# Optimization experiments

Measured on AMD Instinct MI355X. Metric: run time of the kernel, lower is better.

The kernel has to match this reference:

```python
import jax, jax.numpy as jnp
import numpy as np

N_NODES = 5000
N_EDGES = 40000
NUM_ATOM_TYPES = 100
HID = 32            # multiplicity of 0e and 1o in irreps_hidden
EDGE_ATTR_DIM = 8
NUM_BOND_TYPES = 5
OUT_SCALARS = 2 * 6 + 1  # max_charge=6 -> 13x0e
CUTOFF = 5.0
SQRT3 = 1.7320508075688772


def _sh(edge_vec):
    # o3.SphericalHarmonics('1x0e + 1x1o', normalize=True, normalization='component')
    d = jnp.sqrt(jnp.sum(edge_vec * edge_vec, axis=-1) + 1e-12)
    n = edge_vec / d[:, None]
    sh0 = jnp.ones(edge_vec.shape[0], edge_vec.dtype)          # [E]
    sh1 = SQRT3 * n[:, (1, 2, 0)]                              # [E,3], e3nn (y,z,x) order
    return sh0, sh1, d


def _soft_one_hot(d):
    # e3nn.math.soft_one_hot_linspace(d, 0, cutoff, 8, basis='gaussian', cutoff=True)
    values = jnp.linspace(0.0, CUTOFF, EDGE_ATTR_DIM + 2)[1:-1]
    step = CUTOFF / (EDGE_ATTR_DIM + 1)
    diff = (d[:, None] - values[None, :]) / step
    return jnp.exp(-diff * diff) / 1.12


def _mlp(x, W0, b0, W1, b1):
    # ScalarMLP(in, out, hidden=[in], SiLU)
    return jax.nn.silu(x @ W0 + b0) @ W1 + b1


def _tp_init(s, sh0, sh1, w):
    # FCTP(32x0e, 1x0e+1x1o -> 32x0e+32x1o); paths: 0e*0e->0e, 0e*1o->1o
    E = s.shape[0]
    w1 = w[:, : HID * HID].reshape(E, HID, HID)
    w2 = w[:, HID * HID :].reshape(E, HID, HID)
    c = 1.0 / np.sqrt(HID)  # fan-in = 32 per output irrep
    out_s = c * jnp.einsum('eu,euw->ew', s * sh0[:, None], w1)
    out_v = c * jnp.einsum('eu,ei,euw->ewi', s, sh1, w2)
    return out_s, out_v


def _tp_hidden(s, v, sh0, sh1, w):
    # FCTP(32x0e+32x1o, 1x0e+1x1o -> 32x0e+32x1o)
    # path order: 0e*0e->0e, 0e*1o->1o, 1o*0e->1o, 1o*1o->0e
    E = s.shape[0]
    ws = w.reshape(E, 4, HID, HID)
    c = 1.0 / np.sqrt(2 * HID)  # fan-in = 64 per output irrep
    dot = jnp.einsum('eui,ei->eu', v, sh1) / SQRT3  # CG(1,1->0) = delta/sqrt(3)
    out_s = c * (jnp.einsum('eu,euw->ew', s * sh0[:, None], ws[:, 0]) +
                 jnp.einsum('eu,euw->ew', dot, ws[:, 3]))
    out_v = c * (jnp.einsum('eu,ei,euw->ewi', s, sh1, ws[:, 1]) +
                 jnp.einsum('eui,euw->ewi', v * sh0[:, None, None], ws[:, 2]))
    return out_s, out_v


def _edge_tp(s1, v1, s2, v2, sh0, sh1, w):
    # FCTP(64x0e+64x1o (concat of two hidden), 1x0e+1x1o -> 5x0e)
    # blocks in concat order: s_src, v_src, s_dst, v_dst
    E = s1.shape[0]
    ws = w.reshape(E, 4, HID, NUM_BOND_TYPES)
    c = 1.0 / np.sqrt(4 * HID)  # fan-in = 128
    d1 = jnp.einsum('eui,ei->eu', v1, sh1) / SQRT3
    d2 = jnp.einsum('eui,ei->eu', v2, sh1) / SQRT3
    return c * (jnp.einsum('eu,euw->ew', s1 * sh0[:, None], ws[:, 0]) +
                jnp.einsum('eu,euw->ew', d1, ws[:, 1]) +
                jnp.einsum('eu,euw->ew', s2 * sh0[:, None], ws[:, 2]) +
                jnp.einsum('eu,euw->ew', d2, ws[:, 3]))


def _scatter_mean(ms, mv, dst, n):
    cnt = jax.ops.segment_sum(jnp.ones(dst.shape[0], ms.dtype), dst, num_segments=n)
    cnt = jnp.maximum(cnt, 1.0)
    s = jax.ops.segment_sum(ms, dst, num_segments=n) / cnt[:, None]
    v = jax.ops.segment_sum(mv, dst, num_segments=n) / cnt[:, None, None]
    return s, v


def setup_inputs() -> dict:
    key = jax.random.key(0)
    ks = jax.random.split(key, 16)
    def w(k, shape, fan_in):
        return jax.random.normal(k, shape, dtype=jnp.float32) / np.sqrt(fan_in)
    inp = {}
    inp['coordinates'] = jax.random.normal(ks[0], (N_NODES, 3), dtype=jnp.float32) * 1.5
    inp['atom_types'] = jax.random.randint(ks[1], (N_NODES,), 0, NUM_ATOM_TYPES)
    inp['edge_index'] = jax.random.randint(ks[2], (2, N_EDGES), 0, N_NODES)
    inp['atom_embed'] = jax.random.normal(ks[3], (NUM_ATOM_TYPES, HID), dtype=jnp.float32)
    inp['ip_W0'] = w(ks[4], (EDGE_ATTR_DIM, EDGE_ATTR_DIM), EDGE_ATTR_DIM)
    inp['ip_b0'] = jnp.zeros((EDGE_ATTR_DIM,), jnp.float32)
    inp['ip_W1'] = w(ks[5], (EDGE_ATTR_DIM, 2 * HID * HID), EDGE_ATTR_DIM)
    inp['ip_b1'] = jnp.zeros((2 * HID * HID,), jnp.float32)
    inp['ly_W0'] = w(ks[6], (EDGE_ATTR_DIM, EDGE_ATTR_DIM), EDGE_ATTR_DIM)
    inp['ly_b0'] = jnp.zeros((EDGE_ATTR_DIM,), jnp.float32)
    inp['ly_W1'] = w(ks[7], (EDGE_ATTR_DIM, 4 * HID * HID), EDGE_ATTR_DIM)
    inp['ly_b1'] = jnp.zeros((4 * HID * HID,), jnp.float32)
    inp['ly_Ws'] = jax.random.normal(ks[8], (HID, HID), dtype=jnp.float32)
    inp['ly_Wv'] = jax.random.normal(ks[9], (HID, HID), dtype=jnp.float32)
    inp['et_W0'] = w(ks[10], (EDGE_ATTR_DIM, EDGE_ATTR_DIM), EDGE_ATTR_DIM)
    inp['et_b0'] = jnp.zeros((EDGE_ATTR_DIM,), jnp.float32)
    inp['et_W1'] = w(ks[11], (EDGE_ATTR_DIM, 4 * HID * NUM_BOND_TYPES), EDGE_ATTR_DIM)
    inp['et_b1'] = jnp.zeros((4 * HID * NUM_BOND_TYPES,), jnp.float32)
    inp['no_W1'] = jax.random.normal(ks[12], (HID, OUT_SCALARS), dtype=jnp.float32)
    inp['no_W2'] = jax.random.normal(ks[13], (OUT_SCALARS, OUT_SCALARS), dtype=jnp.float32)
    return inp


def reference(coordinates, atom_types, edge_index, atom_embed,
              ip_W0, ip_b0, ip_W1, ip_b1,
              ly_W0, ly_b0, ly_W1, ly_b1, ly_Ws, ly_Wv,
              et_W0, et_b0, et_W1, et_b1, no_W1, no_W2):
    n = coordinates.shape[0]
    src, dst = edge_index[0], edge_index[1]
    edge_vec = coordinates[dst] - coordinates[src]
    sh0, sh1, d = _sh(edge_vec)
    edge_attr = _soft_one_hot(d)                              # [E,8]
    # initial projector: Conv(32x0e -> 32x0e+32x1o)
    s0 = atom_embed[atom_types]                               # [N,32]
    w_ip = _mlp(edge_attr, ip_W0, ip_b0, ip_W1, ip_b1)        # [E,2048]
    ms, mv = _tp_init(s0[src], sh0, sh1, w_ip)
    s, v = _scatter_mean(ms, mv, dst, n)                      # [N,32],[N,32,3]
    # one LinearSelfInteraction(Conv) layer
    w_ly = _mlp(edge_attr, ly_W0, ly_b0, ly_W1, ly_b1)        # [E,4096]
    ms, mv = _tp_hidden(s[src], v[src], sh0, sh1, w_ly)
    cs, cv = _scatter_mean(ms, mv, dst, n)
    lc = 1.0 / np.sqrt(HID)  # e3nn o3.Linear normalization
    s = cs + lc * (s @ ly_Ws)
    v = cv + lc * jnp.einsum('eui,uw->ewi', v, ly_Wv)
    # edge output: FCTP([h_src, h_dst], edge_sh) with radial weights
    w_et = _mlp(edge_attr, et_W0, et_b0, et_W1, et_b1)        # [E,640]
    edge_out = _edge_tp(s[src], v[src], s[dst], v[dst], sh0, sh1, w_et)  # [E,5]
    # node output MLP on detached scalar channel (13x0e)
    sd = jax.lax.stop_gradient(s)
    h = jax.nn.silu(sd @ no_W1 / np.sqrt(HID))
    node_out = h @ no_W2 / np.sqrt(OUT_SCALARS)               # [N,13]
    return edge_out, node_out
```

## Files before the change

kernel.cpp:

```cpp
#include <hip/hip_runtime.h>

#define NN 5000
#define NE 40000

typedef unsigned int u32;
typedef unsigned short u16;
typedef __fp16 h16x2 __attribute__((ext_vector_type(2)));
typedef _Float16 f16x8 __attribute__((ext_vector_type(8)));
typedef __attribute__((ext_vector_type(4))) float f32x4;

union AF { u32 u[4]; f16x8 v; uint4 q; };

__device__ __forceinline__ float siluf(float x) { return x / (1.f + __expf(-x)); }

__device__ __forceinline__ u32 f2bf_u(float f) {
  u32 x = __float_as_uint(f);
  return (x + 0x7FFFu + ((x >> 16) & 1u)) >> 16;
}
__device__ __forceinline__ u16 f2bf(float f) { return (u16)f2bf_u(f); }
__device__ __forceinline__ u32 packbf2(float lo, float hi) {
  return f2bf_u(lo) | (f2bf_u(hi) << 16);
}
__device__ __forceinline__ u32 pkh2(float a, float b) {
  union { h16x2 h; u32 u; } r;
  r.h = __builtin_amdgcn_cvt_pkrtz(a, b);
  return r.u;
}
__device__ __forceinline__ u16 f2h(float v) {
  _Float16 h = (_Float16)v;
  return *(u16*)&h;
}
__device__ __forceinline__ void unpack8(uint4 q, float* f) {
  f[0] = __uint_as_float(q.x << 16); f[1] = __uint_as_float(q.x & 0xFFFF0000u);
  f[2] = __uint_as_float(q.y << 16); f[3] = __uint_as_float(q.y & 0xFFFF0000u);
  f[4] = __uint_as_float(q.z << 16); f[5] = __uint_as_float(q.z & 0xFFFF0000u);
  f[6] = __uint_as_float(q.w << 16); f[7] = __uint_as_float(q.w & 0xFFFF0000u);
}
__device__ __forceinline__ float dot8f(const float* h, const float* w, float init) {
  float a = init;
#pragma unroll
  for (int k = 0; k < 8; k++) a = fmaf(h[k], w[k], a);
  return a;
}
__device__ __forceinline__ void mlp8(const float* ea, const float* __restrict__ W0,
                                     const float* __restrict__ b0, float* h) {
#pragma unroll
  for (int j = 0; j < 8; j++) {
    float a = b0[j];
#pragma unroll
    for (int i = 0; i < 8; i++) a += ea[i] * W0[i*8 + j];
    h[j] = siluf(a);
  }
}
__device__ __forceinline__ AF mkfrag(float hs, const float* s) {
  AF a;
  a.u[0] = pkh2(hs*s[0], hs*s[1]);
  a.u[1] = pkh2(hs*s[2], hs*s[3]);
  a.u[2] = pkh2(hs*s[4], hs*s[5]);
  a.u[3] = pkh2(hs*s[6], hs*s[7]);
  return a;
}

__global__ __launch_bounds__(256) void k_prep(
    const float* __restrict__ ipW1, const float* __restrict__ ipb1,
    const float* __restrict__ lyW1, const float* __restrict__ lyb1,
    u16* __restrict__ ipT, u16* __restrict__ lyT) {
  int b = blockIdx.x;
  if (b < 16) {
    int h = b >> 3;
    int t0 = (b & 7)*2304 + threadIdx.x*9;
#pragma unroll
    for (int j = 0; j < 9; j++) {
      int t = t0 + j;
      int kch = t >> 9, rem = t & 511;
      int col = rem >> 3, kk = rem & 7;
      int k = kch*8 + kk;
      int basec = (h == 0) ? ((col >> 5)*1024 + (col & 31))
                           : ((col < 32) ? (2048 + col) : (3072 + (col - 32)));
      float v = (k < 256) ? lyW1[(k >> 5)*4096 + basec + (k & 31)*32]
                          : lyb1[basec + (k - 256)*32];
      lyT[h*18432 + t] = f2h(v);
    }
  } else {
    int t0 = (b - 16)*2304 + threadIdx.x*9;
#pragma unroll
    for (int j = 0; j < 9; j++) {
      int t = t0 + j;
      int kch = t >> 9, rem = t & 511;
      int col = rem >> 3, kk = rem & 7;
      int k = kch*8 + kk;
      int pth = col >> 5, w = col & 31;
      float v = (k < 256) ? ipW1[(k >> 5)*2048 + pth*1024 + (k & 31)*32 + w]
                          : ipb1[pth*1024 + (k - 256)*32 + w];
      ipT[t] = f2h(v);
    }
  }
}

__global__ __launch_bounds__(256) void k_conv1(
    const float* __restrict__ coords, const int* __restrict__ eidx,
    const float* __restrict__ emb, const int* __restrict__ atype,
    const float* __restrict__ ipW0, const float* __restrict__ ipb0,
    const float* __restrict__ lyW0, const float* __restrict__ lyb0,
    const float* __restrict__ etW0, const float* __restrict__ etb0,
    const u16* __restrict__ ipT,
    float* __restrict__ sh, float* __restrict__ h_ly, float* __restrict__ h_et,
    int* __restrict__ cur, int* __restrict__ perm, u16* __restrict__ msg) {
  int wid = threadIdx.x >> 6, lane = threadIdx.x & 63;
  int tile = blockIdx.x*4 + wid;
  int m = lane & 15, q = lane >> 4;
  int e = tile*16 + m;
  int s = eidx[e], d = eidx[NE + e];
  float vx = coords[d*3+0] - coords[s*3+0];
  float vy = coords[d*3+1] - coords[s*3+1];
  float vz = coords[d*3+2] - coords[s*3+2];
  float dist = sqrtf(vx*vx + vy*vy + vz*vz + 1e-12f);
  float dinv = 1.f / dist;
  const float SQ3 = 1.7320508075688772f;
  float sh0 = SQ3 * vy * dinv;
  float sh1 = SQ3 * vz * dinv;
  float sh2 = SQ3 * vx * dinv;
  int srow = atype[s];
  float ea[8];
  const float step = 5.f / 9.f;
#pragma unroll
  for (int jj = 0; jj < 8; jj++) {
    float diff = (dist - step * (float)(jj+1)) * (9.f / 5.f);
    ea[jj] = __expf(-diff*diff) * (1.f / 1.12f);
  }
  float hip[8], hly[8], het[8];
  mlp8(ea, ipW0, ipb0, hip);
  mlp8(ea, lyW0, lyb0, hly);
  mlp8(ea, etW0, etb0, het);
  if (q == 0) {
    sh[e*3+0] = sh0; sh[e*3+1] = sh1; sh[e*3+2] = sh2;
    { float4 f0 = {hly[0],hly[1],hly[2],hly[3]}, f1 = {hly[4],hly[5],hly[6],hly[7]};
      *(float4*)&h_ly[e*8] = f0; *(float4*)&h_ly[e*8+4] = f1; }
    { float4 f0 = {het[0],het[1],het[2],het[3]}, f1 = {het[4],het[5],het[6],het[7]};
      *(float4*)&h_et[e*8] = f0; *(float4*)&h_et[e*8+4] = f1; }
    int* cp = &cur[d];
    atomicCAS(cp, (int)0xAAAAAAAA, 0);
    int t = atomicAdd(cp, 1);
    if (t < 64) perm[d*64 + t] = e;
  }
  float4 sA = *(const float4*)&emb[srow*32 + q*8];
  float4 sB = *(const float4*)&emb[srow*32 + q*8 + 4];
  float sf[8] = {sA.x,sA.y,sA.z,sA.w,sB.x,sB.y,sB.z,sB.w};
  f32x4 acc0 = {0.f,0.f,0.f,0.f}, acc1 = acc0, acc2 = acc0, acc3 = acc0;
  const float cs = 0.17677669529663687f;
#pragma unroll
  for (int ks = 0; ks < 9; ks++) {
    float hs = (ks < 8) ? hip[ks] : 1.f;
    AF a = mkfrag(hs, sf);
    int c2 = (ks*4 + q)*64;
    AF b0, b1f, b2, b3;
    b0.q  = *(const uint4*)&ipT[(c2 +  0 + m)*8];
    b1f.q = *(const uint4*)&ipT[(c2 + 16 + m)*8];
    b2.q  = *(const uint4*)&ipT[(c2 + 32 + m)*8];
    b3.q  = *(const uint4*)&ipT[(c2 + 48 + m)*8];
    acc0 = __builtin_amdgcn_mfma_f32_16x16x32_f16(a.v, b0.v,  acc0, 0, 0, 0);
    acc1 = __builtin_amdgcn_mfma_f32_16x16x32_f16(a.v, b1f.v, acc1, 0, 0, 0);
    acc2 = __builtin_amdgcn_mfma_f32_16x16x32_f16(a.v, b2.v,  acc2, 0, 0, 0);
    acc3 = __builtin_amdgcn_mfma_f32_16x16x32_f16(a.v, b3.v,  acc3, 0, 0, 0);
  }
#pragma unroll
  for (int r = 0; r < 4; r++) {
    int et = tile*16 + q*4 + r;
    u16* mp = msg + (size_t)et*128;
    mp[m]      = f2bf(cs*acc0[r]);
    mp[16 + m] = f2bf(cs*acc1[r]);
    float s0v = __shfl(sh0, q*4 + r, 64);
    float s1v = __shfl(sh1, q*4 + r, 64);
    float s2v = __shfl(sh2, q*4 + r, 64);
    float m0 = cs*acc2[r], m1 = cs*acc3[r];
    mp[32 +      m] = f2bf(m0*s0v);
    mp[64 +      m] = f2bf(m0*s1v);
    mp[96 +      m] = f2bf(m0*s2v);
    mp[32 + 16 + m] = f2bf(m1*s0v);
    mp[64 + 16 + m] = f2bf(m1*s1v);
    mp[96 + 16 + m] = f2bf(m1*s2v);
  }
}

__global__ __launch_bounds__(256) void k_conv2(
    const float* __restrict__ hE, const float* __restrict__ sh,
    const float* __restrict__ s1, const float* __restrict__ v1soa,
    const int* __restrict__ eidx, const u16* __restrict__ lyT,
    u16* __restrict__ msgA, u16* __restrict__ msgB) {
  int wid = threadIdx.x >> 6, lane = threadIdx.x & 63;
  const bool scalarHalf = blockIdx.x < 625;
  int blk = scalarHalf ? blockIdx.x : blockIdx.x - 625;
  int tile = blk*4 + wid;
  int m = lane & 15, q = lane >> 4;
  const u16* Bg = lyT + (scalarHalf ? 0 : 18432);
  const float c = 0.125f;
  int e = tile*16 + m;
  int srcn = eidx[e];
  float4 hA = *(const float4*)&hE[e*8];
  float4 hB = *(const float4*)&hE[e*8 + 4];
  float hf[8] = {hA.x,hA.y,hA.z,hA.w,hB.x,hB.y,hB.z,hB.w};

  if (scalarHalf) {
    float4 sA = *(const float4*)&s1[srcn*32 + q*8];
    float4 sB = *(const float4*)&s1[srcn*32 + q*8 + 4];
    float sf[8] = {sA.x,sA.y,sA.z,sA.w,sB.x,sB.y,sB.z,sB.w};
    f32x4 acc0 = {0.f,0.f,0.f,0.f}, acc1 = acc0, acc2 = acc0, acc3 = acc0;
#pragma unroll
    for (int ks = 0; ks < 9; ks++) {
      float hs = (ks < 8) ? hf[ks] : 1.f;
      AF a = mkfrag(hs, sf);
      int c2 = (ks*4 + q)*64;
      AF b0, b1f, b2, b3;
      b0.q  = *(const uint4*)&Bg[(c2 +  0 + m)*8];
      b1f.q = *(const uint4*)&Bg[(c2 + 16 + m)*8];
      b2.q  = *(const uint4*)&Bg[(c2 + 32 + m)*8];
      b3.q  = *(const uint4*)&Bg[(c2 + 48 + m)*8];
      acc0 = __builtin_amdgcn_mfma_f32_16x16x32_f16(a.v, b0.v,  acc0, 0, 0, 0);
      acc1 = __builtin_amdgcn_mfma_f32_16x16x32_f16(a.v, b1f.v, acc1, 0, 0, 0);
      acc2 = __builtin_amdgcn_mfma_f32_16x16x32_f16(a.v, b2.v,  acc2, 0, 0, 0);
      acc3 = __builtin_amdgcn_mfma_f32_16x16x32_f16(a.v, b3.v,  acc3, 0, 0, 0);
    }
#pragma unroll
    for (int r = 0; r < 4; r++) {
      int et = tile*16 + q*4 + r;
      u16* mp = msgA + (size_t)et*128;
      mp[m]      = f2bf(c*acc0[r]);
      mp[16 + m] = f2bf(c*acc1[r]);
      float s0v = sh[et*3+0], s1v = sh[et*3+1], s2v = sh[et*3+2];
      float m0 = c*acc2[r], m1 = c*acc3[r];
      mp[32 +      m] = f2bf(m0*s0v);
      mp[64 +      m] = f2bf(m0*s1v);
      mp[96 +      m] = f2bf(m0*s2v);
      mp[32 + 16 + m] = f2bf(m1*s0v);
      mp[64 + 16 + m] = f2bf(m1*s1v);
      mp[96 + 16 + m] = f2bf(m1*s2v);
    }
  } else {
    const float is3 = 0.5773502691896258f;
    float vf[3][8];
#pragma unroll
    for (int i = 0; i < 3; i++) {
      float4 aa = *(const float4*)&v1soa[i*160000 + srcn*32 + q*8];
      float4 bb = *(const float4*)&v1soa[i*160000 + srcn*32 + q*8 + 4];
      vf[i][0]=aa.x; vf[i][1]=aa.y; vf[i][2]=aa.z; vf[i][3]=aa.w;
      vf[i][4]=bb.x; vf[i][5]=bb.y; vf[i][6]=bb.z; vf[i][7]=bb.w;
    }
    float es0 = sh[e*3+0], es1 = sh[e*3+1], es2 = sh[e*3+2];
    float df[8];
#pragma unroll
    for (int j = 0; j < 8; j++)
      df[j] = (vf[0][j]*es0 + vf[1][j]*es1 + vf[2][j]*es2) * is3;
    f32x4 z = {0.f,0.f,0.f,0.f};
    f32x4 aV00 = z, aV01 = z, aV10 = z, aV11 = z, aV20 = z, aV21 = z, aD0 = z, aD1 = z;
#pragma unroll
    for (int ks = 0; ks < 9; ks++) {
      float hs = (ks < 8) ? hf[ks] : 1.f;
      int c2 = (ks*4 + q)*64;
      AF b0, b1f, b2, b3;
      b0.q  = *(const uint4*)&Bg[(c2 +  0 + m)*8];
      b1f.q = *(const uint4*)&Bg[(c2 + 16 + m)*8];
      b2.q  = *(const uint4*)&Bg[(c2 + 32 + m)*8];
      b3.q  = *(const uint4*)&Bg[(c2 + 48 + m)*8];
      AF a0 = mkfrag(hs, vf[0]);
      AF a1 = mkfrag(hs, vf[1]);
      AF a2 = mkfrag(hs, vf[2]);
      AF ad = mkfrag(hs, df);
      aV00 = __builtin_amdgcn_mfma_f32_16x16x32_f16(a0.v, b0.v,  aV00, 0, 0, 0);
      aV01 = __builtin_amdgcn_mfma_f32_16x16x32_f16(a0.v, b1f.v, aV01, 0, 0, 0);
      aV10 = __builtin_amdgcn_mfma_f32_16x16x32_f16(a1.v, b0.v,  aV10, 0, 0, 0);
      aV11 = __builtin_amdgcn_mfma_f32_16x16x32_f16(a1.v, b1f.v, aV11, 0, 0, 0);
      aV20 = __builtin_amdgcn_mfma_f32_16x16x32_f16(a2.v, b0.v,  aV20, 0, 0, 0);
      aV21 = __builtin_amdgcn_mfma_f32_16x16x32_f16(a2.v, b1f.v, aV21, 0, 0, 0);
      aD0  = __builtin_amdgcn_mfma_f32_16x16x32_f16(ad.v, b2.v,  aD0,  0, 0, 0);
      aD1  = __builtin_amdgcn_mfma_f32_16x16x32_f16(ad.v, b3.v,  aD1,  0, 0, 0);
    }
#pragma unroll
    for (int r = 0; r < 4; r++) {
      int et = tile*16 + q*4 + r;
      u16* mp = msgB + (size_t)et*128;
      mp[m]      = f2bf(c*aD0[r]);
      mp[16 + m] = f2bf(c*aD1[r]);
      mp[32 +      m] = f2bf(c*aV00[r]);
      mp[32 + 16 + m] = f2bf(c*aV01[r]);
      mp[64 +      m] = f2bf(c*aV10[r]);
      mp[64 + 16 + m] = f2bf(c*aV11[r]);
      mp[96 +      m] = f2bf(c*aV20[r]);
      mp[96 + 16 + m] = f2bf(c*aV21[r]);
    }
  }
}

__global__ __launch_bounds__(256) void k_gather1(
    const u16* __restrict__ msg, const int* __restrict__ perm,
    const int* __restrict__ cur, float* __restrict__ s1,
    float* __restrict__ v1soa) {
  __shared__ int pe[2][64];
  int ln = threadIdx.x >> 7, c = threadIdx.x & 127;
  int n = blockIdx.x*2 + ln;
  int deg = min(cur[n], 64);
  if (c < 64) pe[ln][c] = perm[n*64 + c];
  __syncthreads();
  float acc = 0.f;
  int j = 0;
  for (; j + 4 <= deg; j += 4) {
    int e0 = pe[ln][j], e1 = pe[ln][j+1], e2 = pe[ln][j+2], e3 = pe[ln][j+3];
    float x0 = __uint_as_float(((u32)msg[(size_t)e0*128 + c]) << 16);
    float x1 = __uint_as_float(((u32)msg[(size_t)e1*128 + c]) << 16);
    float x2 = __uint_as_float(((u32)msg[(size_t)e2*128 + c]) << 16);
    float x3 = __uint_as_float(((u32)msg[(size_t)e3*128 + c]) << 16);
    acc += (x0 + x1) + (x2 + x3);
  }
  for (; j < deg; j++)
    acc += __uint_as_float(((u32)msg[(size_t)pe[ln][j]*128 + c]) << 16);
  acc /= (float)max(deg, 1);
  if (c < 32) s1[n*32 + c] = acc;
  else { int i = (c-32) >> 5, w = (c-32) & 31; v1soa[i*160000 + n*32 + w] = acc; }
}

__global__ __launch_bounds__(256) void k_gather2(
    const u16* __restrict__ msgA, const u16* __restrict__ msgB,
    const int* __restrict__ perm, const int* __restrict__ cur,
    const float* __restrict__ s1, const float* __restrict__ v1soa,
    const float* __restrict__ Ws, const float* __restrict__ Wv,
    const float* __restrict__ noW1, const float* __restrict__ noW2,
    float* __restrict__ s2, float* __restrict__ v2, float* __restrict__ outN) {
  __shared__ int pe[2][64];
  __shared__ float sb[2][32];
  __shared__ float hb[2][13];
  int ln = threadIdx.x >> 7, c = threadIdx.x & 127;
  int n = blockIdx.x*2 + ln;
  int deg = min(cur[n], 64);
  if (c < 64) pe[ln][c] = perm[n*64 + c];
  __syncthreads();
  float acc = 0.f;
  int j = 0;
  for (; j + 4 <= deg; j += 4) {
    int e0 = pe[ln][j], e1 = pe[ln][j+1], e2 = pe[ln][j+2], e3 = pe[ln][j+3];
    float x0 = __uint_as_float(((u32)msgA[(size_t)e0*128 + c]) << 16)
             + __uint_as_float(((u32)msgB[(size_t)e0*128 + c]) << 16);
    float x1 = __uint_as_float(((u32)msgA[(size_t)e1*128 + c]) << 16)
             + __uint_as_float(((u32)msgB[(size_t)e1*128 + c]) << 16);
    float x2 = __uint_as_float(((u32)msgA[(size_t)e2*128 + c]) << 16)
             + __uint_as_float(((u32)msgB[(size_t)e2*128 + c]) << 16);
    float x3 = __uint_as_float(((u32)msgA[(size_t)e3*128 + c]) << 16)
             + __uint_as_float(((u32)msgB[(size_t)e3*128 + c]) << 16);
    acc += (x0 + x1) + (x2 + x3);
  }
  for (; j < deg; j++) {
    int e = pe[ln][j];
    acc += __uint_as_float(((u32)msgA[(size_t)e*128 + c]) << 16)
         + __uint_as_float(((u32)msgB[(size_t)e*128 + c]) << 16);
  }
  acc /= (float)max(deg, 1);
  const float lc = 0.17677669529663687f;
  if (c < 32) {
    float ss = 0.f;
#pragma unroll 8
    for (int u = 0; u < 32; u++) ss += s1[n*32 + u] * Ws[u*32 + c];
    float val = acc + lc*ss;
    s2[n*32 + c] = val;
    sb[ln][c] = val;
  } else {
    int i = (c-32) >> 5, w = (c-32) & 31;
    float sv = 0.f;
#pragma unroll 8
    for (int u = 0; u < 32; u++) sv += v1soa[i*160000 + n*32 + u] * Wv[u*32 + w];
    v2[n*96 + w*3 + i] = acc + lc*sv;
  }
  __syncthreads();
  const float i32 = 0.17677669529663687f;
  if (c < 13) {
    float a = 0.f;
#pragma unroll 8
    for (int u = 0; u < 32; u++) a += sb[ln][u] * noW1[u*13 + c];
    hb[ln][c] = siluf(a * i32);
  }
  __syncthreads();
  const float i13 = 0.2773500981126146f;
  if (c < 13) {
    float a = 0.f;
#pragma unroll
    for (int j2 = 0; j2 < 13; j2++) a += hb[ln][j2] * noW2[j2*13 + c];
    outN[n*13 + c] = a * i13;
  }
}

__global__ __launch_bounds__(256) void k_e3(
    const float* __restrict__ hE, const float* __restrict__ sh,
    const float* __restrict__ s2, const float* __restrict__ v2,
    const int* __restrict__ eidx,
    const float* __restrict__ W1, const float* __restrict__ b1,
    float* __restrict__ out) {
  __shared__ uint4 WQ[640];
  __shared__ float BQ[640];
  for (int t = threadIdx.x; t < 640; t += 256) {
    int u = t & 31, pw = t >> 5, p2 = pw / 5, w = pw - p2*5;
    int col = p2*160 + u*5 + w;
    const float* s = W1 + col;
    uint4 q;
    q.x = packbf2(s[0],      s[640]);
    q.y = packbf2(s[1280],   s[1920]);
    q.z = packbf2(s[2560],   s[3200]);
    q.w = packbf2(s[3840],   s[4480]);
    WQ[t] = q;
    BQ[t] = b1[col];
  }
  __syncthreads();
  const int g = threadIdx.x >> 5, tw = threadIdx.x & 31;
  const float c = 0.08838834764831845f;
  const float is3 = 0.5773502691896258f;
  for (int p = blockIdx.x*8 + g; p*2 < NE; p += gridDim.x*8) {
    int e0 = p*2, e1 = e0 + 1;
    float h0[8], h1[8];
    {
      float4 qa = *(const float4*)&hE[e0*8];
      float4 qb = *(const float4*)&hE[e0*8+4];
      h0[0]=qa.x; h0[1]=qa.y; h0[2]=qa.z; h0[3]=qa.w;
      h0[4]=qb.x; h0[5]=qb.y; h0[6]=qb.z; h0[7]=qb.w;
      float4 qc = *(const float4*)&hE[e1*8];
      float4 qd = *(const float4*)&hE[e1*8+4];
      h1[0]=qc.x; h1[1]=qc.y; h1[2]=qc.z; h1[3]=qc.w;
      h1[4]=qd.x; h1[5]=qd.y; h1[6]=qd.z; h1[7]=qd.w;
    }
    int sA = eidx[e0], dA = eidx[NE+e0];
    int sB = eidx[e1], dB = eidx[NE+e1];
    float sa0 = sh[e0*3+0], sa1 = sh[e0*3+1], sa2 = sh[e0*3+2];
    float sb0 = sh[e1*3+0], sb1 = sh[e1*3+1], sb2 = sh[e1*3+2];
    float c00 = s2[sA*32 + tw];
    float c01 = (v2[sA*96+tw*3+0]*sa0 + v2[sA*96+tw*3+1]*sa1 + v2[sA*96+tw*3+2]*sa2) * is3;
    float c02 = s2[dA*32 + tw];
    float c03 = (v2[dA*96+tw*3+0]*sa0 + v2[dA*96+tw*3+1]*sa1 + v2[dA*96+tw*3+2]*sa2) * is3;
    float c10 = s2[sB*32 + tw];
    float c11 = (v2[sB*96+tw*3+0]*sb0 + v2[sB*96+tw*3+1]*sb1 + v2[sB*96+tw*3+2]*sb2) * is3;
    float c12 = s2[dB*32 + tw];
    float c13 = (v2[dB*96+tw*3+0]*sb0 + v2[dB*96+tw*3+1]*sb1 + v2[dB*96+tw*3+2]*sb2) * is3;
    float part0[5] = {0,0,0,0,0};
    float part1[5] = {0,0,0,0,0};
#pragma unroll
    for (int pp = 0; pp < 4; pp++) {
      float cp0 = (pp==0) ? c00 : (pp==1) ? c01 : (pp==2) ? c02 : c03;
      float cp1 = (pp==0) ? c10 : (pp==1) ? c11 : (pp==2) ? c12 : c13;
#pragma unroll
      for (int w = 0; w < 5; w++) {
        int idx = (pp*5 + w)*32 + tw;
        float f[8];
        unpack8(WQ[idx], f);
        float bv = BQ[idx];
        part0[w] = fmaf(cp0, dot8f(h0, f, bv), part0[w]);
        part1[w] = fmaf(cp1, dot8f(h1, f, bv), part1[w]);
      }
    }
#pragma unroll
    for (int off = 16; off > 0; off >>= 1)
#pragma unroll
      for (int w = 0; w < 5; w++) {
        part0[w] += __shfl_xor(part0[w], off, 32);
        part1[w] += __shfl_xor(part1[w], off, 32);
      }
    float outv = 0.f;
#pragma unroll
    for (int w = 0; w < 5; w++) {
      if (tw == w)     outv = part0[w];
      if (tw == 5 + w) outv = part1[w];
    }
    if (tw < 10) out[e0*5 + tw] = c * outv;
  }
}

extern "C" void kernel_launch(void* const* d_in, const int* in_sizes, int n_in,
                              void* d_out, int out_size, void* d_ws, size_t ws_size,
                              hipStream_t stream) {
  (void)in_sizes; (void)n_in; (void)out_size; (void)ws_size;
  const float* coords = (const float*)d_in[0];
  const int*   atype  = (const int*)d_in[1];
  const int*   eidx   = (const int*)d_in[2];
  const float* emb    = (const float*)d_in[3];
  const float* ipW0 = (const float*)d_in[4];
  const float* ipb0 = (const float*)d_in[5];
  const float* ipW1 = (const float*)d_in[6];
  const float* ipb1 = (const float*)d_in[7];
  const float* lyW0 = (const float*)d_in[8];
  const float* lyb0 = (const float*)d_in[9];
  const float* lyW1 = (const float*)d_in[10];
  const float* lyb1 = (const float*)d_in[11];
  const float* lyWs = (const float*)d_in[12];
  const float* lyWv = (const float*)d_in[13];
  const float* etW0 = (const float*)d_in[14];
  const float* etb0 = (const float*)d_in[15];
  const float* etW1 = (const float*)d_in[16];
  const float* etb1 = (const float*)d_in[17];
  const float* noW1 = (const float*)d_in[18];
  const float* noW2 = (const float*)d_in[19];

  float* ws = (float*)d_ws;
  float* sh    = ws;
  float* h_ly  = ws + 440000;
  float* h_et  = ws + 760000;
  float* s1    = ws + 1240000;
  float* v1soa = ws + 1400000;
  float* s2    = ws + 1880000;
  float* v2    = ws + 2040000;
  int*   cur   = (int*)(ws + 2520000);
  int*   perm  = (int*)(ws + 2525000);
  u16*   msgA  = (u16*)(ws + 2845000);
  u16*   msgB  = (u16*)(ws + 5405000);
  u16*   lyT   = (u16*)(ws + 7965000);
  u16*   ipT   = (u16*)(ws + 7983432);

  float* outE = (float*)d_out;
  float* outN = (float*)d_out + NE*5;

  k_prep<<<24, 256, 0, stream>>>(ipW1, ipb1, lyW1, lyb1, ipT, lyT);
  k_conv1<<<625, 256, 0, stream>>>(coords, eidx, emb, atype,
                                   ipW0, ipb0, lyW0, lyb0, etW0, etb0,
                                   ipT, sh, h_ly, h_et, cur, perm, msgA);
  k_gather1<<<NN/2, 256, 0, stream>>>(msgA, perm, cur, s1, v1soa);
  k_conv2<<<1250, 256, 0, stream>>>(h_ly, sh, s1, v1soa, eidx, lyT, msgA, msgB);
  k_gather2<<<NN/2, 256, 0, stream>>>(msgA, msgB, perm, cur, s1, v1soa,
                                      lyWs, lyWv, noW1, noW2, s2, v2, outN);
  k_e3<<<1024, 256, 0, stream>>>(h_et, sh, s2, v2, eidx, etW1, etb1, outE);
}
```

Measured before the change: 164.9 us.

## Write messages directly into per-destination slots and stage weights in LDS

Conv kernels now write each edge message straight into a dense per-destination slot buffer indexed by (dst, atomic slot), so the gather kernels read contiguous rows without a perm indirection. Message components are interleaved per channel (s, vx, vy, vz) and stored with packed 8-byte writes instead of scattered 2-byte stores. The k_prep launch is removed: each conv block converts its slice of W1/b1 to fp16 in shared memory, which adds per-block redundant conversion work and a large LDS footprint that may limit occupancy. The message buffers grow to NN*64 slots each, so more workspace is touched.

```diff
diff --git a/kernel.cpp b/kernel.cpp
--- a/kernel.cpp
+++ b/kernel.cpp
@@ -17,7 +17,6 @@
   u32 x = __float_as_uint(f);
   return (x + 0x7FFFu + ((x >> 16) & 1u)) >> 16;
 }
-__device__ __forceinline__ u16 f2bf(float f) { return (u16)f2bf_u(f); }
 __device__ __forceinline__ u32 packbf2(float lo, float hi) {
   return f2bf_u(lo) | (f2bf_u(hi) << 16);
 }
@@ -60,42 +59,7 @@
   a.u[3] = pkh2(hs*s[6], hs*s[7]);
   return a;
 }
-
-__global__ __launch_bounds__(256) void k_prep(
-    const float* __restrict__ ipW1, const float* __restrict__ ipb1,
-    const float* __restrict__ lyW1, const float* __restrict__ lyb1,
-    u16* __restrict__ ipT, u16* __restrict__ lyT) {
-  int b = blockIdx.x;
-  if (b < 16) {
-    int h = b >> 3;
-    int t0 = (b & 7)*2304 + threadIdx.x*9;
-#pragma unroll
-    for (int j = 0; j < 9; j++) {
-      int t = t0 + j;
-      int kch = t >> 9, rem = t & 511;
-      int col = rem >> 3, kk = rem & 7;
-      int k = kch*8 + kk;
-      int basec = (h == 0) ? ((col >> 5)*1024 + (col & 31))
-                           : ((col < 32) ? (2048 + col) : (3072 + (col - 32)));
-      float v = (k < 256) ? lyW1[(k >> 5)*4096 + basec + (k & 31)*32]
-                          : lyb1[basec + (k - 256)*32];
-      lyT[h*18432 + t] = f2h(v);
-    }
-  } else {
-    int t0 = (b - 16)*2304 + threadIdx.x*9;
-#pragma unroll
-    for (int j = 0; j < 9; j++) {
-      int t = t0 + j;
-      int kch = t >> 9, rem = t & 511;
-      int col = rem >> 3, kk = rem & 7;
-      int k = kch*8 + kk;
-      int pth = col >> 5, w = col & 31;
-      float v = (k < 256) ? ipW1[(k >> 5)*2048 + pth*1024 + (k & 31)*32 + w]
-                          : ipb1[pth*1024 + (k - 256)*32 + w];
-      ipT[t] = f2h(v);
-    }
-  }
-}
+__device__ __forceinline__ float bf2f(u16 v) { return __uint_as_float(((u32)v) << 16); }
 
 __global__ __launch_bounds__(256) void k_conv1(
     const float* __restrict__ coords, const int* __restrict__ eidx,
@@ -103,9 +67,19 @@
     const float* __restrict__ ipW0, const float* __restrict__ ipb0,
     const float* __restrict__ lyW0, const float* __restrict__ lyb0,
     const float* __restrict__ etW0, const float* __restrict__ etb0,
-    const u16* __restrict__ ipT,
+    const float* __restrict__ ipW1, const float* __restrict__ ipb1,
     float* __restrict__ sh, float* __restrict__ h_ly, float* __restrict__ h_et,
-    int* __restrict__ cur, int* __restrict__ perm, u16* __restrict__ msg) {
+    int* __restrict__ cur, int* __restrict__ slot, u16* __restrict__ msg) {
+  __shared__ __align__(16) u16 B2[18432];
+  {
+    int col = threadIdx.x & 63, pth = col >> 5, w = col & 31;
+    int k0 = (threadIdx.x >> 6) * 72;
+    for (int k = k0; k < k0 + 72; k++) {
+      float v = (k < 256) ? ipW1[(k >> 5)*2048 + pth*1024 + (k & 31)*32 + w]
+                          : ipb1[pth*1024 + (k - 256)*32 + w];
+      B2[((k >> 3)*64 + col)*8 + (k & 7)] = f2h(v);
+    }
+  }
   int wid = threadIdx.x >> 6, lane = threadIdx.x & 63;
   int tile = blockIdx.x*4 + wid;
   int m = lane & 15, q = lane >> 4;
@@ -132,6 +106,7 @@
   mlp8(ea, ipW0, ipb0, hip);
   mlp8(ea, lyW0, lyb0, hly);
   mlp8(ea, etW0, etb0, het);
+  int t = 0;
   if (q == 0) {
     sh[e*3+0] = sh0; sh[e*3+1] = sh1; sh[e*3+2] = sh2;
     { float4 f0 = {hly[0],hly[1],hly[2],hly[3]}, f1 = {hly[4],hly[5],hly[6],hly[7]};
@@ -140,12 +115,13 @@
       *(float4*)&h_et[e*8] = f0; *(float4*)&h_et[e*8+4] = f1; }
     int* cp = &cur[d];
     atomicCAS(cp, (int)0xAAAAAAAA, 0);
-    int t = atomicAdd(cp, 1);
-    if (t < 64) perm[d*64 + t] = e;
+    t = atomicAdd(cp, 1);
+    slot[e] = t;
   }
   float4 sA = *(const float4*)&emb[srow*32 + q*8];
   float4 sB = *(const float4*)&emb[srow*32 + q*8 + 4];
   float sf[8] = {sA.x,sA.y,sA.z,sA.w,sB.x,sB.y,sB.z,sB.w};
+  __syncthreads();
   f32x4 acc0 = {0.f,0.f,0.f,0.f}, acc1 = acc0, acc2 = acc0, acc3 = acc0;
   const float cs = 0.17677669529663687f;
 #pragma unroll
@@ -154,10 +130,10 @@
     AF a = mkfrag(hs, sf);
     int c2 = (ks*4 + q)*64;
     AF b0, b1f, b2, b3;
-    b0.q  = *(const uint4*)&ipT[(c2 +  0 + m)*8];
-    b1f.q = *(const uint4*)&ipT[(c2 + 16 + m)*8];
-    b2.q  = *(const uint4*)&ipT[(c2 + 32 + m)*8];
-    b3.q  = *(const uint4*)&ipT[(c2 + 48 + m)*8];
+    b0.q  = *(const uint4*)&B2[(c2 +  0 + m)*8];
+    b1f.q = *(const uint4*)&B2[(c2 + 16 + m)*8];
+    b2.q  = *(const uint4*)&B2[(c2 + 32 + m)*8];
+    b3.q  = *(const uint4*)&B2[(c2 + 48 + m)*8];
     acc0 = __builtin_amdgcn_mfma_f32_16x16x32_f16(a.v, b0.v,  acc0, 0, 0, 0);
     acc1 = __builtin_amdgcn_mfma_f32_16x16x32_f16(a.v, b1f.v, acc1, 0, 0, 0);
     acc2 = __builtin_amdgcn_mfma_f32_16x16x32_f16(a.v, b2.v,  acc2, 0, 0, 0);
@@ -165,40 +141,79 @@
   }
 #pragma unroll
   for (int r = 0; r < 4; r++) {
-    int et = tile*16 + q*4 + r;
-    u16* mp = msg + (size_t)et*128;
-    mp[m]      = f2bf(cs*acc0[r]);
-    mp[16 + m] = f2bf(cs*acc1[r]);
-    float s0v = __shfl(sh0, q*4 + r, 64);
-    float s1v = __shfl(sh1, q*4 + r, 64);
-    float s2v = __shfl(sh2, q*4 + r, 64);
-    float m0 = cs*acc2[r], m1 = cs*acc3[r];
-    mp[32 +      m] = f2bf(m0*s0v);
-    mp[64 +      m] = f2bf(m0*s1v);
-    mp[96 +      m] = f2bf(m0*s2v);
-    mp[32 + 16 + m] = f2bf(m1*s0v);
-    mp[64 + 16 + m] = f2bf(m1*s1v);
-    mp[96 + 16 + m] = f2bf(m1*s2v);
-  }
+    int L = q*4 + r;
+    int tE = __shfl(t, L, 64);
+    int dn = __shfl(d, L, 64);
+    float s0v = __shfl(sh0, L, 64);
+    float s1v = __shfl(sh1, L, 64);
+    float s2v = __shfl(sh2, L, 64);
+    if (tE < 64) {
+      u16* mp = msg + ((size_t)dn*64 + tE)*128;
+      float m0 = cs*acc2[r], m1 = cs*acc3[r];
+      uint2 p0 = { packbf2(cs*acc0[r], m0*s0v), packbf2(m0*s1v, m0*s2v) };
+      *(uint2*)&mp[m*4] = p0;
+      uint2 p1 = { packbf2(cs*acc1[r], m1*s0v), packbf2(m1*s1v, m1*s2v) };
+      *(uint2*)&mp[64 + m*4] = p1;
+    }
+  }
+}
+
+__global__ __launch_bounds__(256) void k_gather1(
+    const u16* __restrict__ msg, const int* __restrict__ cur,
+    float* __restrict__ s1, float* __restrict__ v1soa) {
+  int ln = threadIdx.x >> 7, c = threadIdx.x & 127;
+  int n = blockIdx.x*2 + ln;
+  int deg = min(cur[n], 64);
+  const u16* base = msg + (size_t)n*64*128 + c;
+  float acc = 0.f;
+  int j = 0;
+  for (; j + 4 <= deg; j += 4) {
+    float x0 = bf2f(base[(j+0)*128]);
+    float x1 = bf2f(base[(j+1)*128]);
+    float x2 = bf2f(base[(j+2)*128]);
+    float x3 = bf2f(base[(j+3)*128]);
+    acc += (x0 + x1) + (x2 + x3);
+  }
+  for (; j < deg; j++) acc += bf2f(base[j*128]);
+  acc /= (float)max(deg, 1);
+  int col = c >> 2, comp = c & 3;
+  if (comp == 0) s1[n*32 + col] = acc;
+  else           v1soa[(comp-1)*160000 + n*32 + col] = acc;
 }
 
 __global__ __launch_bounds__(256) void k_conv2(
     const float* __restrict__ hE, const float* __restrict__ sh,
     const float* __restrict__ s1, const float* __restrict__ v1soa,
-    const int* __restrict__ eidx, const u16* __restrict__ lyT,
+    const int* __restrict__ eidx, const int* __restrict__ slot,
+    const float* __restrict__ lyW1, const float* __restrict__ lyb1,
     u16* __restrict__ msgA, u16* __restrict__ msgB) {
-  int wid = threadIdx.x >> 6, lane = threadIdx.x & 63;
+  __shared__ __align__(16) u16 B2[18432];
   const bool scalarHalf = blockIdx.x < 625;
   int blk = scalarHalf ? blockIdx.x : blockIdx.x - 625;
+  {
+    int col = threadIdx.x & 63;
+    int k0 = (threadIdx.x >> 6) * 72;
+    int basec = scalarHalf ? ((col >> 5)*1024 + (col & 31))
+                           : ((col < 32) ? (2048 + col) : (3072 + (col - 32)));
+    for (int k = k0; k < k0 + 72; k++) {
+      float v = (k < 256) ? lyW1[(k >> 5)*4096 + basec + (k & 31)*32]
+                          : lyb1[basec + (k - 256)*32];
+      B2[((k >> 3)*64 + col)*8 + (k & 7)] = f2h(v);
+    }
+  }
+  int wid = threadIdx.x >> 6, lane = threadIdx.x & 63;
   int tile = blk*4 + wid;
   int m = lane & 15, q = lane >> 4;
-  const u16* Bg = lyT + (scalarHalf ? 0 : 18432);
   const float c = 0.125f;
   int e = tile*16 + m;
   int srcn = eidx[e];
+  int dnv  = eidx[NE + e];
+  int slv  = slot[e];
+  float s0p = sh[e*3+0], s1p = sh[e*3+1], s2p = sh[e*3+2];
   float4 hA = *(const float4*)&hE[e*8];
   float4 hB = *(const float4*)&hE[e*8 + 4];
   float hf[8] = {hA.x,hA.y,hA.z,hA.w,hB.x,hB.y,hB.z,hB.w};
+  __syncthreads();
 
   if (scalarHalf) {
     float4 sA = *(const float4*)&s1[srcn*32 + q*8];
@@ -211,10 +226,10 @@
       AF a = mkfrag(hs, sf);
       int c2 = (ks*4 + q)*64;
       AF b0, b1f, b2, b3;
-      b0.q  = *(const uint4*)&Bg[(c2 +  0 + m)*8];
-      b1f.q = *(const uint4*)&Bg[(c2 + 16 + m)*8];
-      b2.q  = *(const uint4*)&Bg[(c2 + 32 + m)*8];
-      b3.q  = *(const uint4*)&Bg[(c2 + 48 + m)*8];
+      b0.q  = *(const uint4*)&B2[(c2 +  0 + m)*8];
+      b1f.q = *(const uint4*)&B2[(c2 + 16 + m)*8];
+      b2.q  = *(const uint4*)&B2[(c2 + 32 + m)*8];
+      b3.q  = *(const uint4*)&B2[(c2 + 48 + m)*8];
       acc0 = __builtin_amdgcn_mfma_f32_16x16x32_f16(a.v, b0.v,  acc0, 0, 0, 0);
       acc1 = __builtin_amdgcn_mfma_f32_16x16x32_f16(a.v, b1f.v, acc1, 0, 0, 0);
       acc2 = __builtin_amdgcn_mfma_f32_16x16x32_f16(a.v, b2.v,  acc2, 0, 0, 0);
@@ -222,18 +237,20 @@
     }
 #pragma unroll
     for (int r = 0; r < 4; r++) {
-      int et = tile*16 + q*4 + r;
-      u16* mp = msgA + (size_t)et*128;
-      mp[m]      = f2bf(c*acc0[r]);
-      mp[16 + m] = f2bf(c*acc1[r]);
-      float s0v = sh[et*3+0], s1v = sh[et*3+1], s2v = sh[et*3+2];
-      float m0 = c*acc2[r], m1 = c*acc3[r];
-      mp[32 +      m] = f2bf(m0*s0v);
-      mp[64 +      m] = f2bf(m0*s1v);
-      mp[96 +      m] = f2bf(m0*s2v);
-      mp[32 + 16 + m] = f2bf(m1*s0v);
-      mp[64 + 16 + m] = f2bf(m1*s1v);
-      mp[96 + 16 + m] = f2bf(m1*s2v);
+      int L = q*4 + r;
+      int tE = __shfl(slv, L, 64);
+      int dn = __shfl(dnv, L, 64);
+      float s0v = __shfl(s0p, L, 64);
+      float s1v = __shfl(s1p, L, 64);
+      float s2v = __shfl(s2p, L, 64);
+      if (tE < 64) {
+        u16* mp = msgA + ((size_t)dn*64 + tE)*128;
+        float m0 = c*acc2[r], m1 = c*acc3[r];
+        uint2 p0 = { packbf2(c*acc0[r], m0*s0v), packbf2(m0*s1v, m0*s2v) };
+        *(uint2*)&mp[m*4] = p0;
+        uint2 p1 = { packbf2(c*acc1[r], m1*s0v), packbf2(m1*s1v, m1*s2v) };
+        *(uint2*)&mp[64 + m*4] = p1;
+      }
     }
   } else {
     const float is3 = 0.5773502691896258f;
@@ -245,11 +262,10 @@
       vf[i][0]=aa.x; vf[i][1]=aa.y; vf[i][2]=aa.z; vf[i][3]=aa.w;
       vf[i][4]=bb.x; vf[i][5]=bb.y; vf[i][6]=bb.z; vf[i][7]=bb.w;
     }
-    float es0 = sh[e*3+0], es1 = sh[e*3+1], es2 = sh[e*3+2];
     float df[8];
 #pragma unroll
     for (int j = 0; j < 8; j++)
-      df[j] = (vf[0][j]*es0 + vf[1][j]*es1 + vf[2][j]*es2) * is3;
+      df[j] = (vf[0][j]*s0p + vf[1][j]*s1p + vf[2][j]*s2p) * is3;
     f32x4 z = {0.f,0.f,0.f,0.f};
     f32x4 aV00 = z, aV01 = z, aV10 = z, aV11 = z, aV20 = z, aV21 = z, aD0 = z, aD1 = z;
 #pragma unroll
@@ -257,10 +273,10 @@
       float hs = (ks < 8) ? hf[ks] : 1.f;
       int c2 = (ks*4 + q)*64;
       AF b0, b1f, b2, b3;
-      b0.q  = *(const uint4*)&Bg[(c2 +  0 + m)*8];
-      b1f.q = *(const uint4*)&Bg[(c2 + 16 + m)*8];
-      b2.q  = *(const uint4*)&Bg[(c2 + 32 + m)*8];
-      b3.q  = *(const uint4*)&Bg[(c2 + 48 + m)*8];
+      b0.q  = *(const uint4*)&B2[(c2 +  0 + m)*8];
+      b1f.q = *(const uint4*)&B2[(c2 + 16 + m)*8];
+      b2.q  = *(const uint4*)&B2[(c2 + 32 + m)*8];
+      b3.q  = *(const uint4*)&B2[(c2 + 48 + m)*8];
       AF a0 = mkfrag(hs, vf[0]);
       AF a1 = mkfrag(hs, vf[1]);
       AF a2 = mkfrag(hs, vf[2]);
@@ -276,96 +292,60 @@
     }
 #pragma unroll
     for (int r = 0; r < 4; r++) {
-      int et = tile*16 + q*4 + r;
-      u16* mp = msgB + (size_t)et*128;
-      mp[m]      = f2bf(c*aD0[r]);
-      mp[16 + m] = f2bf(c*aD1[r]);
-      mp[32 +      m] = f2bf(c*aV00[r]);
-      mp[32 + 16 + m] = f2bf(c*aV01[r]);
-      mp[64 +      m] = f2bf(c*aV10[r]);
-      mp[64 + 16 + m] = f2bf(c*aV11[r]);
-      mp[96 +      m] = f2bf(c*aV20[r]);
-      mp[96 + 16 + m] = f2bf(c*aV21[r]);
-    }
-  }
-}
-
-__global__ __launch_bounds__(256) void k_gather1(
-    const u16* __restrict__ msg, const int* __restrict__ perm,
-    const int* __restrict__ cur, float* __restrict__ s1,
-    float* __restrict__ v1soa) {
-  __shared__ int pe[2][64];
-  int ln = threadIdx.x >> 7, c = threadIdx.x & 127;
-  int n = blockIdx.x*2 + ln;
-  int deg = min(cur[n], 64);
-  if (c < 64) pe[ln][c] = perm[n*64 + c];
-  __syncthreads();
-  float acc = 0.f;
-  int j = 0;
-  for (; j + 4 <= deg; j += 4) {
-    int e0 = pe[ln][j], e1 = pe[ln][j+1], e2 = pe[ln][j+2], e3 = pe[ln][j+3];
-    float x0 = __uint_as_float(((u32)msg[(size_t)e0*128 + c]) << 16);
-    float x1 = __uint_as_float(((u32)msg[(size_t)e1*128 + c]) << 16);
-    float x2 = __uint_as_float(((u32)msg[(size_t)e2*128 + c]) << 16);
-    float x3 = __uint_as_float(((u32)msg[(size_t)e3*128 + c]) << 16);
-    acc += (x0 + x1) + (x2 + x3);
-  }
-  for (; j < deg; j++)
-    acc += __uint_as_float(((u32)msg[(size_t)pe[ln][j]*128 + c]) << 16);
-  acc /= (float)max(deg, 1);
-  if (c < 32) s1[n*32 + c] = acc;
-  else { int i = (c-32) >> 5, w = (c-32) & 31; v1soa[i*160000 + n*32 + w] = acc; }
+      int L = q*4 + r;
+      int tE = __shfl(slv, L, 64);
+      int dn = __shfl(dnv, L, 64);
+      if (tE < 64) {
+        u16* mp = msgB + ((size_t)dn*64 + tE)*128;
+        uint2 p0 = { packbf2(c*aD0[r], c*aV00[r]), packbf2(c*aV10[r], c*aV20[r]) };
+        *(uint2*)&mp[m*4] = p0;
+        uint2 p1 = { packbf2(c*aD1[r], c*aV01[r]), packbf2(c*aV11[r], c*aV21[r]) };
+        *(uint2*)&mp[64 + m*4] = p1;
+      }
+    }
+  }
 }
 
 __global__ __launch_bounds__(256) void k_gather2(
     const u16* __restrict__ msgA, const u16* __restrict__ msgB,
-    const int* __restrict__ perm, const int* __restrict__ cur,
+    const int* __restrict__ cur,
     const float* __restrict__ s1, const float* __restrict__ v1soa,
     const float* __restrict__ Ws, const float* __restrict__ Wv,
     const float* __restrict__ noW1, const float* __restrict__ noW2,
     float* __restrict__ s2, float* __restrict__ v2, float* __restrict__ outN) {
-  __shared__ int pe[2][64];
   __shared__ float sb[2][32];
   __shared__ float hb[2][13];
   int ln = threadIdx.x >> 7, c = threadIdx.x & 127;
   int n = blockIdx.x*2 + ln;
   int deg = min(cur[n], 64);
-  if (c < 64) pe[ln][c] = perm[n*64 + c];
-  __syncthreads();
+  const u16* bA = msgA + (size_t)n*64*128 + c;
+  const u16* bB = msgB + (size_t)n*64*128 + c;
   float acc = 0.f;
   int j = 0;
   for (; j + 4 <= deg; j += 4) {
-    int e0 = pe[ln][j], e1 = pe[ln][j+1], e2 = pe[ln][j+2], e3 = pe[ln][j+3];
-    float x0 = __uint_as_float(((u32)msgA[(size_t)e0*128 + c]) << 16)
-             + __uint_as_float(((u32)msgB[(size_t)e0*128 + c]) << 16);
-    float x1 = __uint_as_float(((u32)msgA[(size_t)e1*128 + c]) << 16)
-             + __uint_as_float(((u32)msgB[(size_t)e1*128 + c]) << 16);
-    float x2 = __uint_as_float(((u32)msgA[(size_t)e2*128 + c]) << 16)
-             + __uint_as_float(((u32)msgB[(size_t)e2*128 + c]) << 16);
-    float x3 = __uint_as_float(((u32)msgA[(size_t)e3*128 + c]) << 16)
-             + __uint_as_float(((u32)msgB[(size_t)e3*128 + c]) << 16);
+    float x0 = bf2f(bA[(j+0)*128]) + bf2f(bB[(j+0)*128]);
+    float x1 = bf2f(bA[(j+1)*128]) + bf2f(bB[(j+1)*128]);
+    float x2 = bf2f(bA[(j+2)*128]) + bf2f(bB[(j+2)*128]);
+    float x3 = bf2f(bA[(j+3)*128]) + bf2f(bB[(j+3)*128]);
     acc += (x0 + x1) + (x2 + x3);
   }
-  for (; j < deg; j++) {
-    int e = pe[ln][j];
-    acc += __uint_as_float(((u32)msgA[(size_t)e*128 + c]) << 16)
-         + __uint_as_float(((u32)msgB[(size_t)e*128 + c]) << 16);
-  }
+  for (; j < deg; j++) acc += bf2f(bA[j*128]) + bf2f(bB[j*128]);
   acc /= (float)max(deg, 1);
   const float lc = 0.17677669529663687f;
-  if (c < 32) {
+  int col = c >> 2, comp = c & 3;
+  if (comp == 0) {
     float ss = 0.f;
 #pragma unroll 8
-    for (int u = 0; u < 32; u++) ss += s1[n*32 + u] * Ws[u*32 + c];
+    for (int u = 0; u < 32; u++) ss += s1[n*32 + u] * Ws[u*32 + col];
     float val = acc + lc*ss;
-    s2[n*32 + c] = val;
-    sb[ln][c] = val;
+    s2[n*32 + col] = val;
+    sb[ln][col] = val;
   } else {
-    int i = (c-32) >> 5, w = (c-32) & 31;
+    int i = comp - 1;
     float sv = 0.f;
 #pragma unroll 8
-    for (int u = 0; u < 32; u++) sv += v1soa[i*160000 + n*32 + u] * Wv[u*32 + w];
-    v2[n*96 + w*3 + i] = acc + lc*sv;
+    for (int u = 0; u < 32; u++) sv += v1soa[i*160000 + n*32 + u] * Wv[u*32 + col];
+    v2[n*96 + col*3 + i] = acc + lc*sv;
   }
   __syncthreads();
   const float i32 = 0.17677669529663687f;
@@ -494,29 +474,27 @@
 
   float* ws = (float*)d_ws;
   float* sh    = ws;
-  float* h_ly  = ws + 440000;
-  float* h_et  = ws + 760000;
-  float* s1    = ws + 1240000;
-  float* v1soa = ws + 1400000;
-  float* s2    = ws + 1880000;
-  float* v2    = ws + 2040000;
-  int*   cur   = (int*)(ws + 2520000);
-  int*   perm  = (int*)(ws + 2525000);
-  u16*   msgA  = (u16*)(ws + 2845000);
-  u16*   msgB  = (u16*)(ws + 5405000);
-  u16*   lyT   = (u16*)(ws + 7965000);
-  u16*   ipT   = (u16*)(ws + 7983432);
+  float* h_ly  = ws + 120000;
+  float* h_et  = ws + 440000;
+  float* s1    = ws + 760000;
+  float* v1soa = ws + 920000;
+  float* s2    = ws + 1400000;
+  float* v2    = ws + 1560000;
+  int*   cur   = (int*)(ws + 2040000);
+  int*   slot  = (int*)(ws + 2045000);
+  u16*   msgA  = (u16*)(ws + 2085000);
+  u16*   msgB  = (u16*)(ws + 22565000);
 
   float* outE = (float*)d_out;
   float* outN = (float*)d_out + NE*5;
 
-  k_prep<<<24, 256, 0, stream>>>(ipW1, ipb1, lyW1, lyb1, ipT, lyT);
   k_conv1<<<625, 256, 0, stream>>>(coords, eidx, emb, atype,
                                    ipW0, ipb0, lyW0, lyb0, etW0, etb0,
-                                   ipT, sh, h_ly, h_et, cur, perm, msgA);
-  k_gather1<<<NN/2, 256, 0, stream>>>(msgA, perm, cur, s1, v1soa);
-  k_conv2<<<1250, 256, 0, stream>>>(h_ly, sh, s1, v1soa, eidx, lyT, msgA, msgB);
-  k_gather2<<<NN/2, 256, 0, stream>>>(msgA, msgB, perm, cur, s1, v1soa,
+                                   ipW1, ipb1, sh, h_ly, h_et, cur, slot, msgA);
+  k_gather1<<<NN/2, 256, 0, stream>>>(msgA, cur, s1, v1soa);
+  k_conv2<<<1250, 256, 0, stream>>>(h_ly, sh, s1, v1soa, eidx, slot,
+                                    lyW1, lyb1, msgA, msgB);
+  k_gather2<<<NN/2, 256, 0, stream>>>(msgA, msgB, cur, s1, v1soa,
                                       lyWs, lyWv, noW1, noW2, s2, v2, outN);
   k_e3<<<1024, 256, 0, stream>>>(h_et, sh, s2, v2, eidx, etW1, etb1, outE);
 }
```

After: 182.0 us. 10.4% more time.
